# Kernel tuning notes

Hardware: AMD Instinct MI355X
Metric: run time of the kernel (lower is better)

## Reference

```python
import jax, jax.numpy as jnp
import numpy as np

C = 32          # d_model / channels
D_STATE = 32
D_CONV = 4
EXPAND = 2
D_INNER = EXPAND * C          # 64
DT_RANK = (C + 15) // 16      # ceil(32/16) = 2
EPS = 1e-5


def _conv2d(x, w, b):
    # x: (B,C,H,W), w: (O,I,3,3), stride 1, padding 1 (torch Conv2d)
    y = jax.lax.conv_general_dilated(
        x, w, window_strides=(1, 1), padding=[(1, 1), (1, 1)],
        dimension_numbers=("NCHW", "OIHW", "NCHW"))
    return y + b[None, :, None, None]


def _silu(x):
    return x * jax.nn.sigmoid(x)


def _mamba(xs, in_proj_w, conv1d_w, conv1d_b, x_proj_w, dt_proj_w, dt_proj_b,
           A_log, Dp, out_proj_w):
    # xs: (B, L, C)
    xz = xs @ in_proj_w.T                       # (B, L, 2*D_INNER)
    xm, z = jnp.split(xz, 2, axis=-1)           # each (B, L, D_INNER)

    # causal depthwise conv1d along L (torch: padding=d_conv-1 then [..., :L])
    xc = xm.transpose(0, 2, 1)                  # (B, D_INNER, L)
    xc = jax.lax.conv_general_dilated(
        xc, conv1d_w, window_strides=(1,), padding=[(D_CONV - 1, 0)],
        dimension_numbers=("NCH", "OIH", "NCH"),
        feature_group_count=D_INNER)
    xm = _silu((xc + conv1d_b[None, :, None]).transpose(0, 2, 1))  # (B,L,D_INNER)

    x_dbl = xm @ x_proj_w.T                     # (B, L, DT_RANK + 2*D_STATE)
    dt = x_dbl[..., :DT_RANK]
    Bm = x_dbl[..., DT_RANK:DT_RANK + D_STATE]  # (B, L, N)
    Cm = x_dbl[..., DT_RANK + D_STATE:]         # (B, L, N)

    delta = jax.nn.softplus(dt @ dt_proj_w.T + dt_proj_b)  # (B, L, D_INNER)
    A = -jnp.exp(A_log)                                     # (D_INNER, N)

    deltaA = jnp.exp(delta[..., None] * A)                           # (B,L,D,N)
    deltaBx = delta[..., None] * Bm[:, :, None, :] * xm[..., None]   # (B,L,D,N)

    def combine(c1, c2):
        a1, b1 = c1
        a2, b2 = c2
        return a1 * a2, a2 * b1 + b2

    # parallel linear recurrence h_t = deltaA_t * h_{t-1} + deltaBx_t
    _, hstate = jax.lax.associative_scan(combine, (deltaA, deltaBx), axis=1)

    y = jnp.einsum("bldn,bln->bld", hstate, Cm) + xm * Dp
    y = y * _silu(z)
    return y @ out_proj_w.T                     # (B, L, C)


def setup_inputs() -> dict:
    key = jax.random.key(0)
    ks = jax.random.split(key, 16)
    s = 0.02
    inp = {
        "x": jax.random.normal(ks[0], (4, C, 64, 64), dtype=jnp.float32),
        "conv1_w": jax.random.normal(ks[1], (2 * C, C, 3, 3), jnp.float32) * s,
        "conv1_b": jnp.zeros((2 * C,), jnp.float32),
        "conv2_w": jax.random.normal(ks[2], (C, 2 * C, 3, 3), jnp.float32) * s,
        "conv2_b": jnp.zeros((C,), jnp.float32),
        "ln_g": jnp.ones((C,), jnp.float32),
        "ln_b": jnp.zeros((C,), jnp.float32),
        "in_proj_w": jax.random.normal(ks[3], (2 * D_INNER, C), jnp.float32) * s,
        "conv1d_w": jax.random.normal(ks[4], (D_INNER, 1, D_CONV), jnp.float32) * 0.1,
        "conv1d_b": jnp.zeros((D_INNER,), jnp.float32),
        "x_proj_w": jax.random.normal(ks[5], (DT_RANK + 2 * D_STATE, D_INNER), jnp.float32) * s,
        "dt_proj_w": jax.random.normal(ks[6], (D_INNER, DT_RANK), jnp.float32) * 0.1,
        "dt_proj_b": jax.random.normal(ks[7], (D_INNER,), jnp.float32) * 0.1 - 4.0,
        "A_log": jnp.log(jnp.tile(jnp.arange(1, D_STATE + 1, dtype=jnp.float32), (D_INNER, 1))),
        "Dp": jnp.ones((D_INNER,), jnp.float32),
        "out_proj_w": jax.random.normal(ks[8], (C, D_INNER), jnp.float32) * s,
        "smooth_w": jax.random.normal(ks[9], (C, C, 3, 3), jnp.float32) * s,
        "smooth_b": jnp.zeros((C,), jnp.float32),
    }
    return inp


def reference(x, conv1_w, conv1_b, conv2_w, conv2_b, ln_g, ln_b,
              in_proj_w, conv1d_w, conv1d_b, x_proj_w, dt_proj_w, dt_proj_b,
              A_log, Dp, out_proj_w, smooth_w, smooth_b):
    b, c, h, w = x.shape
    # convb residual
    t = jax.nn.relu(_conv2d(x, conv1_w, conv1_b))
    x = _conv2d(t, conv2_w, conv2_b) + x
    # reshape (b,c,h,w) -> (b, h*w, c) row-major (faithful to torch .reshape)
    xs = x.reshape(b, -1, c)
    # LayerNorm over last dim
    mu = jnp.mean(xs, axis=-1, keepdims=True)
    var = jnp.mean(jnp.square(xs - mu), axis=-1, keepdims=True)
    xs = (xs - mu) * jax.lax.rsqrt(var + EPS) * ln_g + ln_b
    # Mamba block
    y = _mamba(xs, in_proj_w, conv1d_w, conv1d_b, x_proj_w, dt_proj_w,
               dt_proj_b, A_log, Dp, out_proj_w)
    y = y.transpose(0, 2, 1).reshape(b, c, h, w)
    return _conv2d(y, smooth_w, smooth_b)
```

## Files before the change

### kernel.cpp

```cpp
#include <hip/hip_runtime.h>
#include <math.h>

#define SEQL 4096
#define L2E 1.44269504088896340736f

#if defined(__has_builtin)
#if __has_builtin(__builtin_amdgcn_exp2f)
#define FAST_EXP2(x) __builtin_amdgcn_exp2f(x)
#endif
#endif
#ifndef FAST_EXP2
#define FAST_EXP2(x) exp2f(x)
#endif

__device__ __forceinline__ float sigmoid_f(float x){ return 1.0f/(1.0f+expf(-x)); }

template<int CI, int CO, int COW, bool RELU, bool RES>
__global__ __launch_bounds__(256) void conv3x3_k(const float* __restrict__ in,
    const float* __restrict__ wgt, const float* __restrict__ bias,
    const float* __restrict__ res, float* __restrict__ out)
{
  constexpr int NST = CI / 32;
  __shared__ __align__(16) float tin[32][4][72];
  const int tid  = threadIdx.x;
  const int lane = tid & 63;
  const int ty   = tid >> 6;
  const int tyu  = __builtin_amdgcn_readfirstlane(ty);
  const int h0   = blockIdx.x * 2;
  const int co0  = blockIdx.y * (4*COW) + tyu*COW;
  const int b    = blockIdx.z;

  float acc[2][COW];
  #pragma unroll
  for (int rr=0;rr<2;++rr)
    #pragma unroll
    for (int u=0;u<COW;++u) acc[rr][u] = 0.0f;

  for (int st=0; st<NST; ++st){
    const int cig = st*32;
    if (st) __syncthreads();
    #pragma unroll
    for (int k=0;k<8;++k){
      int i   = tid + (k<<8);
      int ci  = i >> 6;
      int rem = i & 63;
      int row = rem >> 4;
      int w4  = (rem & 15) << 2;
      int h   = h0 - 1 + row;
      float4 v = make_float4(0.f,0.f,0.f,0.f);
      if (h>=0 && h<64)
        v = *(const float4*)(in + ((size_t)(b*CI+cig+ci)*64 + h)*64 + w4);
      *(float4*)&tin[ci][row][4+w4] = v;
      if (w4 == 0)  tin[ci][row][3]  = 0.0f;
      if (w4 == 60) tin[ci][row][68] = 0.0f;
    }
    __syncthreads();
    #pragma unroll 4
    for (int ci=0; ci<32; ++ci){
      float rv[4][3];
      #pragma unroll
      for (int r=0;r<4;++r)
        #pragma unroll
        for (int c=0;c<3;++c)
          rv[r][c] = tin[ci][r][3+lane+c];
      #pragma unroll
      for (int u=0;u<COW;++u){
        const float* wp = wgt + ((size_t)(co0+u)*CI + cig + ci)*9;
        #pragma unroll
        for (int j=0;j<3;++j){
          float w0 = wp[3*j+0], w1 = wp[3*j+1], w2 = wp[3*j+2];
          #pragma unroll
          for (int rr=0;rr<2;++rr){
            acc[rr][u] = fmaf(rv[rr+j][0], w0, acc[rr][u]);
            acc[rr][u] = fmaf(rv[rr+j][1], w1, acc[rr][u]);
            acc[rr][u] = fmaf(rv[rr+j][2], w2, acc[rr][u]);
          }
        }
      }
    }
  }

  #pragma unroll
  for (int u=0;u<COW;++u){
    const float bv = bias[co0+u];
    #pragma unroll
    for (int rr=0;rr<2;++rr){
      float s = acc[rr][u] + bv;
      size_t ob = ((size_t)(b*CO+co0+u)*64 + h0+rr)*64 + lane;
      if constexpr (RES)  s += res[ob];
      if constexpr (RELU) s = fmaxf(s, 0.0f);
      out[ob] = s;
    }
  }
}

__global__ __launch_bounds__(1024, 4) void mamba_in_k(const float* __restrict__ x2,
    const float* __restrict__ g, const float* __restrict__ be,
    const float* __restrict__ Wip, const float* __restrict__ cw,
    const float* __restrict__ cb, const float* __restrict__ Wxp,
    const float* __restrict__ Wdt, const float* __restrict__ bdt,
    const float* __restrict__ A_log,
    float* __restrict__ xm2, float* __restrict__ szb, float* __restrict__ dlt,
    float* __restrict__ Bm, float* __restrict__ Cm,
    float* __restrict__ cA, float* __restrict__ cH)
{
  __shared__ __align__(16) float xn[68][37];
  __shared__ __align__(16) float xm[64][68];
  __shared__ __align__(16) float xtT[64][68];
  __shared__ __align__(16) float xd[64][67];
  float (*xbT)[68] = reinterpret_cast<float(*)[68]>(&xn[0][0]);
  const int tid = threadIdx.x, lane = tid & 63, ty = tid >> 6;
  const int tyu = __builtin_amdgcn_readfirstlane(ty);
  const int bi = blockIdx.x >> 6;
  const int l0 = (blockIdx.x & 63) << 6;

  {
    const int row = tid >> 3, sub = tid & 7;
    if (row < 67){
      const int tok = l0 - 3 + row;
      const int c0 = sub << 2;
      if (tok >= 0){
        float4 f = *(const float4*)(x2 + (size_t)bi*131072 + (size_t)tok*32 + c0);
        float s = (f.x+f.y)+(f.z+f.w);
        s += __shfl_xor(s,1); s += __shfl_xor(s,2); s += __shfl_xor(s,4);
        const float mu = s * 0.03125f;
        float dx=f.x-mu, dy=f.y-mu, dz=f.z-mu, dw=f.w-mu;
        float q = (dx*dx+dy*dy)+(dz*dz+dw*dw);
        q += __shfl_xor(q,1); q += __shfl_xor(q,2); q += __shfl_xor(q,4);
        const float rstd = 1.0f/sqrtf(q*0.03125f + 1e-5f);
        float4 gv = *(const float4*)(g  + c0);
        float4 bv = *(const float4*)(be + c0);
        xn[row][c0+0] = dx*rstd*gv.x + bv.x;
        xn[row][c0+1] = dy*rstd*gv.y + bv.y;
        xn[row][c0+2] = dz*rstd*gv.z + bv.z;
        xn[row][c0+3] = dw*rstd*gv.w + bv.w;
      } else {
        xn[row][c0+0]=0.0f; xn[row][c0+1]=0.0f;
        xn[row][c0+2]=0.0f; xn[row][c0+3]=0.0f;
      }
    }
  }
  __syncthreads();

  if (ty < 8){
    const int d0 = tyu*8;
    float xvA[32];
    #pragma unroll
    for (int c=0;c<32;++c) xvA[c] = xn[lane][c];
    #pragma unroll
    for (int jj=0;jj<8;++jj){
      const float4* wr = (const float4*)(Wip + (d0+jj)*32);
      float a = 0.0f;
      #pragma unroll
      for (int c4=0;c4<8;++c4){
        float4 w = wr[c4];
        a = fmaf(xvA[c4*4+0], w.x, a);
        a = fmaf(xvA[c4*4+1], w.y, a);
        a = fmaf(xvA[c4*4+2], w.z, a);
        a = fmaf(xvA[c4*4+3], w.w, a);
      }
      xm[d0+jj][lane] = a;
    }
    if (lane < 3){
      float xvB[32];
      #pragma unroll
      for (int c=0;c<32;++c) xvB[c] = xn[64+lane][c];
      #pragma unroll
      for (int jj=0;jj<8;++jj){
        const float4* wr = (const float4*)(Wip + (d0+jj)*32);
        float a = 0.0f;
        #pragma unroll
        for (int c4=0;c4<8;++c4){
          float4 w = wr[c4];
          a = fmaf(xvB[c4*4+0], w.x, a);
          a = fmaf(xvB[c4*4+1], w.y, a);
          a = fmaf(xvB[c4*4+2], w.z, a);
          a = fmaf(xvB[c4*4+3], w.w, a);
        }
        xm[d0+jj][64+lane] = a;
      }
    }
  } else {
    const int d0z = (tyu-8)*8;
    float xvC[32];
    #pragma unroll
    for (int c=0;c<32;++c) xvC[c] = xn[lane+3][c];
    #pragma unroll
    for (int jj=0;jj<8;++jj){
      const float4* wr = (const float4*)(Wip + (64+d0z+jj)*32);
      float a = 0.0f;
      #pragma unroll
      for (int c4=0;c4<8;++c4){
        float4 w = wr[c4];
        a = fmaf(xvC[c4*4+0], w.x, a);
        a = fmaf(xvC[c4*4+1], w.y, a);
        a = fmaf(xvC[c4*4+2], w.z, a);
        a = fmaf(xvC[c4*4+3], w.w, a);
      }
      szb[((size_t)(bi*64+d0z+jj))*SEQL + l0 + lane] = a * sigmoid_f(a);
    }
  }
  __syncthreads();

  #pragma unroll
  for (int jj=0;jj<4;++jj){
    int d = tyu*4 + jj;
    float4 w = *(const float4*)(cw + d*4);
    float a = xm[d][lane]*w.x + xm[d][lane+1]*w.y
            + xm[d][lane+2]*w.z + xm[d][lane+3]*w.w + cb[d];
    float s = a * sigmoid_f(a);
    xtT[d][lane] = s;
    xm2[((size_t)(bi*64+d))*SEQL + l0 + lane] = s;
  }
  __syncthreads();

  {
    float xv[64];
    #pragma unroll
    for (int c=0;c<64;++c) xv[c] = xtT[c][lane];
    for (int j=tyu; j<66; j+=16){
      const float4* wr = (const float4*)(Wxp + j*64);
      float a = 0.0f;
      #pragma unroll
      for (int c4=0;c4<16;++c4){
        float4 w = wr[c4];
        a = fmaf(xv[c4*4+0], w.x, a);
        a = fmaf(xv[c4*4+1], w.y, a);
        a = fmaf(xv[c4*4+2], w.z, a);
        a = fmaf(xv[c4*4+3], w.w, a);
      }
      xd[lane][j] = a;
    }
  }
  __syncthreads();

  {
    float dt0 = xd[lane][0], dt1 = xd[lane][1];
    #pragma unroll
    for (int k=0;k<4;++k){
      int d2 = tyu*4 + k;
      float2 wd = *(const float2*)(Wdt + d2*2);
      float v = dt0*wd.x + dt1*wd.y + bdt[d2];
      float sp = fmaxf(v,0.0f) + log1pf(expf(-fabsf(v)));
      dlt[((size_t)(bi*64+d2))*SEQL + l0 + lane] = sp;
      xm[d2][lane] = sp;
    }
    const int which = tyu >> 3, gq = tyu & 7;
    float* dst = which ? Cm : Bm;
    size_t base = ((size_t)bi*SEQL + l0 + lane)*32 + gq*4;
    const int s2 = 2 + which*32;
    float4 f0;
    f0.x = xd[lane][s2+gq+ 0]; f0.y = xd[lane][s2+gq+ 8];
    f0.z = xd[lane][s2+gq+16]; f0.w = xd[lane][s2+gq+24];
    *(float4*)(dst + base) = f0;
    if (!which){
      xbT[gq     ][lane] = f0.x;
      xbT[gq +  8][lane] = f0.y;
      xbT[gq + 16][lane] = f0.z;
      xbT[gq + 24][lane] = f0.w;
    }
  }
  __syncthreads();

  {
    const int d  = tid >> 4;
    const int gg = tid & 15;
    const int chunk = blockIdx.x & 63;
    const int bd = bi*64 + d;
    float Av0 = -expf(A_log[d*32 + gg     ]) * L2E;
    float Av1 = -expf(A_log[d*32 + gg + 16]) * L2E;
    float h0=0.0f, h1=0.0f, aP0=1.0f, aP1=1.0f;
    #pragma unroll 2
    for (int t0=0;t0<64;t0+=4){
      float4 dl4 = *(const float4*)&xm [d    ][t0];
      float4 xs4 = *(const float4*)&xtT[d    ][t0];
      float4 b04 = *(const float4*)&xbT[gg   ][t0];
      float4 b14 = *(const float4*)&xbT[gg+16][t0];
      #pragma unroll
      for (int k=0;k<4;++k){
        float dlv = (k==0)? dl4.x : (k==1)? dl4.y : (k==2)? dl4.z : dl4.w;
        float xsv = (k==0)? xs4.x : (k==1)? xs4.y : (k==2)? xs4.z : xs4.w;
        float bv0 = (k==0)? b04.x : (k==1)? b04.y : (k==2)? b04.z : b04.w;
        float bv1 = (k==0)? b14.x : (k==1)? b14.y : (k==2)? b14.z : b14.w;
        float m  = dlv * xsv;
        float a0 = FAST_EXP2(dlv*Av0);
        float a1 = FAST_EXP2(dlv*Av1);
        h0 = fmaf(a0, h0, m*bv0);  aP0 *= a0;
        h1 = fmaf(a1, h1, m*bv1);  aP1 *= a1;
      }
    }
    size_t base = ((size_t)bd*64 + chunk)*32;
    cA[base + gg] = aP0; cA[base + gg + 16] = aP1;
    cH[base + gg] = h0;  cH[base + gg + 16] = h1;
  }
}

__global__ __launch_bounds__(256) void scan_p2(const float* __restrict__ dlt,
    const float* __restrict__ xssm, const float* __restrict__ Bm,
    const float* __restrict__ Cm, const float* __restrict__ A_log,
    const float* __restrict__ Dp, const float* __restrict__ sz,
    const float* __restrict__ cA, const float* __restrict__ cHs,
    float* __restrict__ yt)
{
  __shared__ float pre[32][34];
  const int tid = threadIdx.x;
  const int grp = blockIdx.x & 1;
  const int bd  = blockIdx.x >> 1;
  const int b = bd >> 6, d = bd & 63;
  const int c0 = grp << 5;

  if (tid < 32){
    const float* pa = cA  + (size_t)bd*2048 + tid;
    const float* ph = cHs + (size_t)bd*2048 + tid;
    float hrun = 0.0f;
    if (grp){
      #pragma unroll 4
      for (int c=0;c<32;++c)
        hrun = fmaf(pa[c*32], hrun, ph[c*32]);
    }
    #pragma unroll 4
    for (int k=0;k<32;++k){
      pre[tid][k] = hrun;
      hrun = fmaf(pa[(c0+k)*32], hrun, ph[(c0+k)*32]);
    }
  }
  __syncthreads();

  const int lc = tid >> 3, gg = tid & 7;
  const int chunk = c0 + lc;
  const int l0 = chunk << 6;
  const float Dv = Dp[d];
  float Av2[4], h[4];
  #pragma unroll
  for (int j=0;j<4;++j){
    Av2[j] = -expf(A_log[d*32 + gg + 8*j]) * L2E;
    h[j] = pre[gg + 8*j][lc];
  }
  const float* del = dlt  + (size_t)bd*SEQL + l0;
  const float* xp  = xssm + (size_t)bd*SEQL + l0;
  const float* szp = sz   + (size_t)bd*SEQL + l0;
  const float* Bp  = Bm + ((size_t)b*SEQL + l0)*32 + gg*4;
  const float* Cp  = Cm + ((size_t)b*SEQL + l0)*32 + gg*4;
  float* yp = yt + (size_t)bd*SEQL + l0;

  for (int i0=0;i0<64;i0+=16){
    float4 y4[4];
    #pragma unroll
    for (int s=0;s<4;++s){
      const int ib = i0 + s*4;
      float4 d4 = *(const float4*)(del+ib);
      float4 x4 = *(const float4*)(xp +ib);
      float4 s4 = *(const float4*)(szp+ib);
      #pragma unroll
      for (int t=0;t<4;++t){
        float dl = (t==0)? d4.x : (t==1)? d4.y : (t==2)? d4.z : d4.w;
        float xl = (t==0)? x4.x : (t==1)? x4.y : (t==2)? x4.z : x4.w;
        float sl = (t==0)? s4.x : (t==1)? s4.y : (t==2)? s4.z : s4.w;
        float4 bv = *(const float4*)(Bp + (ib+t)*32);
        float4 cv = *(const float4*)(Cp + (ib+t)*32);
        float a0 = FAST_EXP2(dl*Av2[0]); h[0] = fmaf(a0, h[0], dl*bv.x*xl);
        float a1 = FAST_EXP2(dl*Av2[1]); h[1] = fmaf(a1, h[1], dl*bv.y*xl);
        float a2 = FAST_EXP2(dl*Av2[2]); h[2] = fmaf(a2, h[2], dl*bv.z*xl);
        float a3 = FAST_EXP2(dl*Av2[3]); h[3] = fmaf(a3, h[3], dl*bv.w*xl);
        float v = fmaf(h[3], cv.w, fmaf(h[2], cv.z, fmaf(h[1], cv.y, h[0]*cv.x)));
        v += __shfl_xor(v,1); v += __shfl_xor(v,2); v += __shfl_xor(v,4);
        float yv = fmaf(xl, Dv, v) * sl;
        if      (t==0) y4[s].x = yv;
        else if (t==1) y4[s].y = yv;
        else if (t==2) y4[s].z = yv;
        else           y4[s].w = yv;
      }
    }
    if (gg < 4){
      float4 w = (gg==0) ? y4[0] : (gg==1) ? y4[1] : (gg==2) ? y4[2] : y4[3];
      *(float4*)(yp + i0 + gg*4) = w;
    }
  }
}

__global__ __launch_bounds__(512) void outproj_k(const float* __restrict__ yt,
    const float* __restrict__ Wout, float* __restrict__ ym)
{
  __shared__ float ys[64][67];
  const int tid = threadIdx.x, lane = tid & 63, ty = tid >> 6;
  const int tyu = __builtin_amdgcn_readfirstlane(ty);
  const int bi = blockIdx.x >> 6;
  const int l0 = (blockIdx.x & 63) << 6;
  for (int r=ty; r<64; r+=8)
    ys[lane][r] = yt[((size_t)(bi*64+r))*SEQL + l0 + lane];
  __syncthreads();
  float yv[64];
  #pragma unroll
  for (int c=0;c<64;++c) yv[c] = ys[lane][c];
  #pragma unroll
  for (int jj=0;jj<4;++jj){
    int j = tyu*4 + jj;
    const float4* wr = (const float4*)(Wout + j*64);
    float acc = 0.0f;
    #pragma unroll
    for (int c4=0;c4<16;++c4){
      float4 w = wr[c4];
      acc = fmaf(yv[c4*4+0], w.x, acc);
      acc = fmaf(yv[c4*4+1], w.y, acc);
      acc = fmaf(yv[c4*4+2], w.z, acc);
      acc = fmaf(yv[c4*4+3], w.w, acc);
    }
    ym[((size_t)(bi*32+j))*SEQL + l0 + lane] = acc;
  }
}

extern "C" void kernel_launch(void* const* d_in, const int* in_sizes, int n_in,
                              void* d_out, int out_size, void* d_ws, size_t ws_size,
                              hipStream_t stream) {
  const float* x        = (const float*)d_in[0];
  const float* conv1_w  = (const float*)d_in[1];
  const float* conv1_b  = (const float*)d_in[2];
  const float* conv2_w  = (const float*)d_in[3];
  const float* conv2_b  = (const float*)d_in[4];
  const float* ln_g     = (const float*)d_in[5];
  const float* ln_b     = (const float*)d_in[6];
  const float* in_proj_w= (const float*)d_in[7];
  const float* conv1d_w = (const float*)d_in[8];
  const float* conv1d_b = (const float*)d_in[9];
  const float* x_proj_w = (const float*)d_in[10];
  const float* dt_proj_w= (const float*)d_in[11];
  const float* dt_proj_b= (const float*)d_in[12];
  const float* A_log    = (const float*)d_in[13];
  const float* Dp       = (const float*)d_in[14];
  const float* out_proj_w=(const float*)d_in[15];
  const float* smooth_w = (const float*)d_in[16];
  const float* smooth_b = (const float*)d_in[17];
  float* out = (float*)d_out;

  float* ws = (float*)d_ws;
  float* t      = ws;
  float* x2     = t      + 1048576;
  float* xm2    = x2     + 524288;
  float* szb    = xm2    + 1048576;
  float* dlt    = szb    + 1048576;
  float* Bmat   = dlt    + 1048576;
  float* Cmat   = Bmat   + 524288;
  float* yt     = Cmat   + 524288;
  float* ym     = yt     + 1048576;
  float* cA     = t;
  float* cH     = t + 524288;

  conv3x3_k<32,64,8,true ,false><<<dim3(32,2,4), 256, 0, stream>>>(x,  conv1_w, conv1_b, nullptr, t);
  conv3x3_k<64,32,4,false,true ><<<dim3(32,2,4), 256, 0, stream>>>(t,  conv2_w, conv2_b, x,       x2);
  mamba_in_k  <<<256, 1024, 0, stream>>>(x2, ln_g, ln_b, in_proj_w, conv1d_w, conv1d_b,
                                         x_proj_w, dt_proj_w, dt_proj_b, A_log,
                                         xm2, szb, dlt, Bmat, Cmat, cA, cH);
  scan_p2     <<<512, 256, 0, stream>>>(dlt, xm2, Bmat, Cmat, A_log, Dp, szb, cA, cH, yt);
  outproj_k   <<<256, 512, 0, stream>>>(yt, out_proj_w, ym);
  conv3x3_k<32,32,4,false,false><<<dim3(32,2,4), 256, 0, stream>>>(ym, smooth_w, smooth_b, nullptr, out);
}
```

Before: 232.4 us.

## Retile 3x3 conv to one output row per block with all input channels staged

The 3x3 conv kernel now computes one output row per block with 512 threads, one wave per output-channel group, so all output channels are covered in a single block. All input channels are staged into shared memory at once, which removes the multi-stage loop and its extra barrier and avoids reading the same input twice across output-channel blocks. In exchange each output row now reads three input rows, so vertical reuse is lower than with two rows per block. Each weight load also feeds half as many FMAs, and shared-memory use grows to about 55KB for the 64-channel case.

```diff
diff --git a/kernel.cpp b/kernel.cpp
--- a/kernel.cpp
+++ b/kernel.cpp
@@ -16,81 +16,68 @@
 __device__ __forceinline__ float sigmoid_f(float x){ return 1.0f/(1.0f+expf(-x)); }
 
 template<int CI, int CO, int COW, bool RELU, bool RES>
-__global__ __launch_bounds__(256) void conv3x3_k(const float* __restrict__ in,
+__global__ __launch_bounds__(512, 2) void conv3x3_k(const float* __restrict__ in,
     const float* __restrict__ wgt, const float* __restrict__ bias,
     const float* __restrict__ res, float* __restrict__ out)
 {
-  constexpr int NST = CI / 32;
-  __shared__ __align__(16) float tin[32][4][72];
+  __shared__ __align__(16) float tin[CI][3][72];
   const int tid  = threadIdx.x;
   const int lane = tid & 63;
   const int ty   = tid >> 6;
   const int tyu  = __builtin_amdgcn_readfirstlane(ty);
-  const int h0   = blockIdx.x * 2;
-  const int co0  = blockIdx.y * (4*COW) + tyu*COW;
-  const int b    = blockIdx.z;
-
-  float acc[2][COW];
-  #pragma unroll
-  for (int rr=0;rr<2;++rr)
-    #pragma unroll
-    for (int u=0;u<COW;++u) acc[rr][u] = 0.0f;
-
-  for (int st=0; st<NST; ++st){
-    const int cig = st*32;
-    if (st) __syncthreads();
-    #pragma unroll
-    for (int k=0;k<8;++k){
-      int i   = tid + (k<<8);
-      int ci  = i >> 6;
-      int rem = i & 63;
-      int row = rem >> 4;
-      int w4  = (rem & 15) << 2;
-      int h   = h0 - 1 + row;
-      float4 v = make_float4(0.f,0.f,0.f,0.f);
-      if (h>=0 && h<64)
-        v = *(const float4*)(in + ((size_t)(b*CI+cig+ci)*64 + h)*64 + w4);
-      *(float4*)&tin[ci][row][4+w4] = v;
-      if (w4 == 0)  tin[ci][row][3]  = 0.0f;
-      if (w4 == 60) tin[ci][row][68] = 0.0f;
-    }
-    __syncthreads();
-    #pragma unroll 4
-    for (int ci=0; ci<32; ++ci){
-      float rv[4][3];
-      #pragma unroll
-      for (int r=0;r<4;++r)
-        #pragma unroll
-        for (int c=0;c<3;++c)
-          rv[r][c] = tin[ci][r][3+lane+c];
-      #pragma unroll
-      for (int u=0;u<COW;++u){
-        const float* wp = wgt + ((size_t)(co0+u)*CI + cig + ci)*9;
-        #pragma unroll
-        for (int j=0;j<3;++j){
-          float w0 = wp[3*j+0], w1 = wp[3*j+1], w2 = wp[3*j+2];
-          #pragma unroll
-          for (int rr=0;rr<2;++rr){
-            acc[rr][u] = fmaf(rv[rr+j][0], w0, acc[rr][u]);
-            acc[rr][u] = fmaf(rv[rr+j][1], w1, acc[rr][u]);
-            acc[rr][u] = fmaf(rv[rr+j][2], w2, acc[rr][u]);
-          }
-        }
+  const int h0   = blockIdx.x;
+  const int b    = blockIdx.y;
+  const int co0  = tyu*COW;
+
+  constexpr int NF4 = CI*48;
+  #pragma unroll
+  for (int k=0; k<NF4/512; ++k){
+    int i   = tid + (k<<9);
+    int ci  = i / 48;
+    int rem = i - ci*48;
+    int row = rem >> 4;
+    int w4  = (rem & 15) << 2;
+    int h   = h0 - 1 + row;
+    float4 v = make_float4(0.f,0.f,0.f,0.f);
+    if (h>=0 && h<64)
+      v = *(const float4*)(in + ((size_t)(b*CI+ci)*64 + h)*64 + w4);
+    *(float4*)&tin[ci][row][4+w4] = v;
+    if (w4 == 0)  tin[ci][row][3]  = 0.0f;
+    if (w4 == 60) tin[ci][row][68] = 0.0f;
+  }
+  __syncthreads();
+
+  float acc[COW];
+  #pragma unroll
+  for (int u=0;u<COW;++u) acc[u] = 0.0f;
+
+  #pragma unroll 2
+  for (int ci=0; ci<CI; ++ci){
+    float rv[3][3];
+    #pragma unroll
+    for (int r=0;r<3;++r)
+      #pragma unroll
+      for (int c=0;c<3;++c)
+        rv[r][c] = tin[ci][r][3+lane+c];
+    #pragma unroll
+    for (int u=0;u<COW;++u){
+      const float* wp = wgt + ((size_t)(co0+u)*CI + ci)*9;
+      #pragma unroll
+      for (int r=0;r<3;++r){
+        acc[u] = fmaf(rv[r][0], wp[3*r+0], acc[u]);
+        acc[u] = fmaf(rv[r][1], wp[3*r+1], acc[u]);
+        acc[u] = fmaf(rv[r][2], wp[3*r+2], acc[u]);
       }
     }
   }
 
   #pragma unroll
   for (int u=0;u<COW;++u){
-    const float bv = bias[co0+u];
-    #pragma unroll
-    for (int rr=0;rr<2;++rr){
-      float s = acc[rr][u] + bv;
-      size_t ob = ((size_t)(b*CO+co0+u)*64 + h0+rr)*64 + lane;
-      if constexpr (RES)  s += res[ob];
-      if constexpr (RELU) s = fmaxf(s, 0.0f);
-      out[ob] = s;
-    }
+    float s = acc[u] + bias[co0+u];
+    size_t ob = ((size_t)(b*CO+co0+u)*64 + h0)*64 + lane;
+    if constexpr (RES)  s += res[ob];
+    if constexpr (RELU) s = fmaxf(s, 0.0f);
+    out[ob] = s;
   }
 }
 
@@ -445,12 +432,12 @@
   float* cA     = t;
   float* cH     = t + 524288;
 
-  conv3x3_k<32,64,8,true ,false><<<dim3(32,2,4), 256, 0, stream>>>(x,  conv1_w, conv1_b, nullptr, t);
-  conv3x3_k<64,32,4,false,true ><<<dim3(32,2,4), 256, 0, stream>>>(t,  conv2_w, conv2_b, x,       x2);
+  conv3x3_k<32,64,8,true ,false><<<dim3(64,4), 512, 0, stream>>>(x,  conv1_w, conv1_b, nullptr, t);
+  conv3x3_k<64,32,4,false,true ><<<dim3(64,4), 512, 0, stream>>>(t,  conv2_w, conv2_b, x,       x2);
   mamba_in_k  <<<256, 1024, 0, stream>>>(x2, ln_g, ln_b, in_proj_w, conv1d_w, conv1d_b,
                                          x_proj_w, dt_proj_w, dt_proj_b, A_log,
                                          xm2, szb, dlt, Bmat, Cmat, cA, cH);
   scan_p2     <<<512, 256, 0, stream>>>(dlt, xm2, Bmat, Cmat, A_log, Dp, szb, cA, cH, yt);
   outproj_k   <<<256, 512, 0, stream>>>(yt, out_proj_w, ym);
-  conv3x3_k<32,32,4,false,false><<<dim3(32,2,4), 256, 0, stream>>>(ym, smooth_w, smooth_b, nullptr, out);
+  conv3x3_k<32,32,4,false,false><<<dim3(64,4), 512, 0, stream>>>(ym, smooth_w, smooth_b, nullptr, out);
 }
```

New measurement: 219.4 us. -5.6%, faster.
